# Performance work log

Measured on AMD Instinct MI355X. Metric: run time of the kernel, lower is better.

Reference implementation:

```python
import jax, jax.numpy as jnp
import numpy as np

NUM_GRAPHS = 4
N_NODES = 50000
N_EDGES = 800000
D_IN = 64
D_HID = 64
D_OUT = 64


def setup_inputs() -> dict:
    key = jax.random.key(0)
    ks = jax.random.split(key, 8)
    x = jax.random.normal(ks[0], (NUM_GRAPHS, N_NODES, D_IN), dtype=jnp.float32)
    edge_index = jax.random.randint(ks[1], (NUM_GRAPHS, 2, N_EDGES), 0, N_NODES, dtype=jnp.int64)
    s = 0.05
    W_l1 = jax.random.normal(ks[2], (NUM_GRAPHS, D_IN, D_HID), dtype=jnp.float32) * s
    W_r1 = jax.random.normal(ks[3], (NUM_GRAPHS, D_IN, D_HID), dtype=jnp.float32) * s
    b1 = jax.random.normal(ks[4], (NUM_GRAPHS, D_HID), dtype=jnp.float32) * s
    W_l2 = jax.random.normal(ks[5], (NUM_GRAPHS, D_HID, D_OUT), dtype=jnp.float32) * s
    W_r2 = jax.random.normal(ks[6], (NUM_GRAPHS, D_HID, D_OUT), dtype=jnp.float32) * s
    b2 = jax.random.normal(ks[7], (NUM_GRAPHS, D_OUT), dtype=jnp.float32) * s
    return {"x": x, "edge_index": edge_index, "W_l1": W_l1, "W_r1": W_r1,
            "b1": b1, "W_l2": W_l2, "W_r2": W_r2, "b2": b2}


def _sage_conv(x, src, dst, W_l, W_r, b):
    # PyG SAGEConv (aggr='mean', root_weight=True): mean(x[src] -> dst) @ W_l + b + x @ W_r
    n = x.shape[0]
    msgs = x[src]                                            # [E, d] irregular gather
    agg = jax.ops.segment_sum(msgs, dst, num_segments=n)     # [N, d]
    deg = jax.ops.segment_sum(jnp.ones((src.shape[0],), x.dtype), dst, num_segments=n)
    mean = agg / jnp.maximum(deg, 1.0)[:, None]              # empty neighborhoods -> 0
    return mean @ W_l + b + x @ W_r


def _per_graph(x, edge_index, W_l1, W_r1, b1, W_l2, W_r2, b2):
    src, dst = edge_index[0], edge_index[1]
    h = jax.nn.elu(_sage_conv(x, src, dst, W_l1, W_r1, b1))
    return jax.nn.elu(_sage_conv(h, src, dst, W_l2, W_r2, b2))


def reference(x, edge_index, W_l1, W_r1, b1, W_l2, W_r2, b2):
    out = jax.vmap(_per_graph)(x, edge_index, W_l1, W_r1, b1, W_l2, W_r2, b2)  # [G, N, out]
    return out.reshape(-1, out.shape[-1])  # concat along node dim -> [G*N, out]
```

## Files before the change

kernel.cpp:

```cpp
#include <hip/hip_runtime.h>
#include <hip/hip_bf16.h>
#include <math.h>

#define NG 4
#define NN 50000
#define NE 800000
#define DD 64
#define CAP 64
#define NT 64
#define NTILE 391
#define NTG (2 * NTILE)
#define RCAP 1536
#define CPAD 16
#define PBLK 128
#define CHUNK (NE / PBLK)
#define LBINS 392
#define BCAP 20

typedef __attribute__((ext_vector_type(8))) short short8;
typedef __attribute__((ext_vector_type(4))) float float4v;

__device__ __forceinline__ unsigned short f2b(float f) {
    union { __hip_bfloat16 h; unsigned short u; } cv;
    cv.h = __float2bfloat16(f);
    return cv.u;
}
__device__ __forceinline__ float b2f(unsigned short u) {
    union { unsigned short u; __hip_bfloat16 h; } cv;
    cv.u = u;
    return __bfloat162float(cv.h);
}

__global__ void init_kernel(const int* __restrict__ ei, int* __restrict__ flags) {
    __shared__ alignas(16) unsigned short A[16 * 32];
    __shared__ unsigned short B[32 * 16];
    int t = threadIdx.x;
    int any_nonzero = 0;
    for (int i = t; i < 128; i += 64) any_nonzero |= ei[2 * i + 1];
    unsigned long long nz = __ballot(any_nonzero != 0);
    int is64 = (nz == 0ULL) ? 1 : 0;
    for (int i = t; i < 512; i += 64) {
        int r = i >> 5, k = i & 31;
        A[i] = f2b((float)(((r * 5 + k * 3) & 31) - 15));
        int kk = i >> 4, c = i & 15;
        B[i] = f2b((float)(((kk * 7 + c * 11) & 31) - 15));
    }
    __syncthreads();
    short8 a = *(const short8*)&A[(t & 15) * 32 + (t >> 4) * 8];
    int c = t & 15, kb = (t >> 4) * 8;
    short8 b;
    for (int j = 0; j < 8; ++j) b[j] = (short)B[(kb + j) * 16 + c];
    float4v acc = {0.f, 0.f, 0.f, 0.f};
    acc = __builtin_amdgcn_mfma_f32_16x16x32_bf16(a, b, acc, 0, 0, 0);
    int ok = 1;
    for (int reg = 0; reg < 4; ++reg) {
        int row = (t >> 4) * 4 + reg;
        float ref = 0.f;
        for (int k = 0; k < 32; ++k)
            ref += (float)(((row * 5 + k * 3) & 31) - 15) *
                   (float)(((k * 7 + c * 11) & 31) - 15);
        if (acc[reg] != ref) ok = 0;
    }
    unsigned long long vote = __ballot(ok);
    if (t == 0) flags[0] = is64 | ((vote == ~0ULL) ? 2 : 0);
}

__device__ __forceinline__ int nt_idx(const int* __restrict__ ei, long pos, int is64) {
    return is64 ? __builtin_nontemporal_load(ei + 2 * pos)
                : __builtin_nontemporal_load(ei + pos);
}

__global__ void partition_kernel(const int* __restrict__ ei, const int* __restrict__ flags,
                                 int* __restrict__ bcnt, unsigned int* __restrict__ part) {
    __shared__ int lcnt[LBINS];
    __shared__ int basev[LBINS];
    __shared__ unsigned int lbuf[LBINS * BCAP];

    int is64 = flags[0] & 1;
    int s = blockIdx.x & 7;
    int g = s >> 1;
    int lo = (s & 1) * (NN / 2), hi = lo + (NN / 2);
    int rbase0 = lo >> 6;
    int bsl = blockIdx.x >> 3;
    int e0 = bsl * CHUNK, e1 = e0 + CHUNK;
    long ebase = (long)g * 2 * NE;

    for (int i = threadIdx.x; i < LBINS; i += 256) lcnt[i] = 0;
    __syncthreads();

    for (int e = e0 + threadIdx.x; e < e1; e += 256) {
        int d = nt_idx(ei, ebase + NE + e, is64);
        int sc = nt_idx(ei, ebase + e, is64);
        if (d >= lo && d < hi) {
            int lb = (d >> 6) - rbase0;
            unsigned int pk = ((unsigned int)d << 16) | (unsigned int)(sc & 0xffff);
            int pos = atomicAdd(&lcnt[lb], 1);
            if (pos < BCAP) {
                lbuf[lb * BCAP + pos] = pk;
            } else {
                int gp = atomicAdd(&bcnt[(g * NTG + (d >> 6)) * CPAD], 1);
                if (gp < RCAP) part[(long)(g * NTG + (d >> 6)) * RCAP + gp] = pk;
            }
        }
    }
    __syncthreads();

    for (int r = threadIdx.x; r < LBINS; r += 256) {
        int c = lcnt[r]; c = c < BCAP ? c : BCAP;
        basev[r] = c ? atomicAdd(&bcnt[(g * NTG + rbase0 + r) * CPAD], c) : 0;
    }
    __syncthreads();

    int w = threadIdx.x >> 6, hw = (threadIdx.x >> 5) & 1, l32 = threadIdx.x & 31;
    for (int r = w * 2 + hw; r < LBINS; r += 8) {
        int c = lcnt[r]; c = c < BCAP ? c : BCAP;
        int b = basev[r];
        if (l32 < c && b + l32 < RCAP)
            part[(long)(g * NTG + rbase0 + r) * RCAP + b + l32] = lbuf[r * BCAP + l32];
    }
}

__global__ void convert_kernel(const float* __restrict__ x, unsigned short* __restrict__ xb) {
    long total = (long)NG * NN * DD / 4;
    long stride = (long)gridDim.x * blockDim.x;
    const float4* src = (const float4*)x;
    unsigned long long* dst = (unsigned long long*)xb;
    for (long i = (long)blockIdx.x * blockDim.x + threadIdx.x; i < total; i += stride) {
        float4 v = src[i];
        unsigned long long p = (unsigned long long)f2b(v.x)
                             | ((unsigned long long)f2b(v.y) << 16)
                             | ((unsigned long long)f2b(v.z) << 32)
                             | ((unsigned long long)f2b(v.w) << 48);
        dst[i] = p;
    }
}

template <int LAYER>
__launch_bounds__(256, 6)
__global__ void sage_mfma_kernel(const unsigned short* __restrict__ xin,
                                 const int* __restrict__ bcnt,
                                 const unsigned int* __restrict__ part,
                                 const float* __restrict__ Wl, const float* __restrict__ Wr,
                                 const float* __restrict__ bias, void* __restrict__ outp,
                                 const int* __restrict__ flags) {
    if (!(flags[0] & 2)) return;
    __shared__ alignas(16) unsigned short sWT[2 * DD * DD];
    __shared__ alignas(16) unsigned short sM[NT * DD];
    __shared__ int cnt_lds[NT];

    int s = blockIdx.x & 7, tb = blockIdx.x >> 3;
    int g = s >> 1;
    int tile = (s & 1) * NTILE + tb;
    int base = tile * NT;
    long gn0 = (long)g * NN;

    if (threadIdx.x < NT) cnt_lds[threadIdx.x] = 0;

    for (int i = threadIdx.x; i < 1024; i += 256) {
        int col = i & 63, ko = (i >> 6) & 7, m = i >> 9;
        const float* Wsrc = (m == 0 ? Wl : Wr) + (long)g * DD * DD;
        short8 t;
#pragma unroll
        for (int j = 0; j < 8; ++j)
            t[j] = (short)f2b(Wsrc[(ko * 8 + j) * DD + col]);
        *(short8*)&sWT[m * DD * DD + col * DD + ((ko * 8) ^ ((col & 7) << 3))] = t;
    }
    __syncthreads();

    int rc = bcnt[(g * NTG + tile) * CPAD];
    int rcount = rc < RCAP ? rc : RCAP;
    const unsigned int* reg = part + (long)(g * NTG + tile) * RCAP;
    for (int i = threadIdx.x; i < rcount; i += 256) {
        unsigned int p = reg[i];
        int dl = (p >> 16) & 63;
        int pos = atomicAdd(&cnt_lds[dl], 1);
        if (pos < CAP) sM[dl * DD + pos] = (unsigned short)(p & 0xffffu);
    }
    __syncthreads();

    int lane = threadIdx.x & 63;
    int w = threadIdx.x >> 6;

#pragma unroll 1
    for (int j = 0; j < 16; ++j) {
        int rl = w * 16 + j;
        int node = base + rl;
        int ne = cnt_lds[rl];
        int nuse = ne < CAP ? ne : CAP;
        int msrc = (int)sM[rl * DD + lane];
        float mean = 0.f;
        if (node < NN) {
            float s0 = 0.f, s1 = 0.f, s2 = 0.f, s3 = 0.f;
            int e = 0;
            for (; e + 4 <= nuse; e += 4) {
                int a0 = __shfl(msrc, e), a1 = __shfl(msrc, e + 1);
                int a2 = __shfl(msrc, e + 2), a3 = __shfl(msrc, e + 3);
                s0 += b2f(xin[(gn0 + a0) * DD + lane]);
                s1 += b2f(xin[(gn0 + a1) * DD + lane]);
                s2 += b2f(xin[(gn0 + a2) * DD + lane]);
                s3 += b2f(xin[(gn0 + a3) * DD + lane]);
            }
            if (e < nuse) {
                int r = nuse - e;
                int a0 = __shfl(msrc, e);
                int a1 = __shfl(msrc, r > 1 ? e + 1 : e);
                int a2 = __shfl(msrc, r > 2 ? e + 2 : e);
                float v0 = b2f(xin[(gn0 + a0) * DD + lane]);
                float v1 = b2f(xin[(gn0 + a1) * DD + lane]);
                float v2 = b2f(xin[(gn0 + a2) * DD + lane]);
                s0 += v0;
                if (r > 1) s1 += v1;
                if (r > 2) s2 += v2;
            }
            mean = ((s0 + s1) + (s2 + s3)) / fmaxf((float)ne, 1.f);
        }
        sM[rl * DD + (lane ^ ((rl & 7) << 3))] = f2b(mean);
    }

    int arow = w * 16 + (lane & 15);
    int kb = (lane >> 4) * 8;
    int selfrow = base + arow; if (selfrow > NN - 1) selfrow = NN - 1;
    short8 am[2], ax[2];
#pragma unroll
    for (int ss = 0; ss < 2; ++ss) {
        int f0 = (kb + 32 * ss) ^ ((arow & 7) << 3);
        am[ss] = *(const short8*)&sM[arow * DD + f0];
        ax[ss] = *(const short8*)&xin[(gn0 + selfrow) * DD + kb + 32 * ss];
    }

    float4v acc[4];
#pragma unroll
    for (int c = 0; c < 4; ++c) {
        float b = bias[g * DD + c * 16 + (lane & 15)];
        acc[c] = {b, b, b, b};
    }
#pragma unroll
    for (int c = 0; c < 4; ++c) {
        int col = c * 16 + (lane & 15);
        int cswz = (col & 7) << 3;
#pragma unroll
        for (int ss = 0; ss < 2; ++ss) {
            short8 bl = *(const short8*)&sWT[0 * DD * DD + col * DD + ((kb + 32 * ss) ^ cswz)];
            acc[c] = __builtin_amdgcn_mfma_f32_16x16x32_bf16(am[ss], bl, acc[c], 0, 0, 0);
        }
#pragma unroll
        for (int ss = 0; ss < 2; ++ss) {
            short8 br = *(const short8*)&sWT[1 * DD * DD + col * DD + ((kb + 32 * ss) ^ cswz)];
            acc[c] = __builtin_amdgcn_mfma_f32_16x16x32_bf16(ax[ss], br, acc[c], 0, 0, 0);
        }
    }

    int q = lane >> 4, cl = lane & 15;
#pragma unroll
    for (int c = 0; c < 4; ++c) {
        int col = c * 16 + cl;
#pragma unroll
        for (int r = 0; r < 4; ++r) {
            int grow = base + w * 16 + q * 4 + r;
            if (grow >= NN) continue;
            float v = acc[c][r];
            v = v > 0.f ? v : expm1f(v);
            if (LAYER == 0)
                ((unsigned short*)outp)[(gn0 + grow) * DD + col] = f2b(v);
            else
                ((float*)outp)[(gn0 + grow) * DD + col] = v;
        }
    }
}

template <int LAYER>
__global__ void fallback_kernel(const unsigned short* __restrict__ xin,
                                const int* __restrict__ bcnt,
                                const unsigned int* __restrict__ part,
                                const float* __restrict__ Wl, const float* __restrict__ Wr,
                                const float* __restrict__ bias, void* __restrict__ outp,
                                const int* __restrict__ flags) {
    if (flags[0] & 2) return;
    __shared__ float sWl[DD * DD];
    __shared__ float sWr[DD * DD];
    __shared__ float sb[DD];
    __shared__ unsigned short bk[NT * CAP];
    __shared__ int cnt_lds[NT];

    int s = blockIdx.x & 7, tb = blockIdx.x >> 3;
    int g = s >> 1;
    int tile = (s & 1) * NTILE + tb;
    int base = tile * NT;
    long gn0 = (long)g * NN;

    if (threadIdx.x < NT) cnt_lds[threadIdx.x] = 0;
    for (int i = threadIdx.x; i < DD * DD; i += blockDim.x) {
        sWl[i] = Wl[(long)g * DD * DD + i];
        sWr[i] = Wr[(long)g * DD * DD + i];
    }
    if (threadIdx.x < DD) sb[threadIdx.x] = bias[g * DD + threadIdx.x];
    __syncthreads();

    int rc = bcnt[(g * NTG + tile) * CPAD];
    int rcount = rc < RCAP ? rc : RCAP;
    const unsigned int* reg = part + (long)(g * NTG + tile) * RCAP;
    for (int i = threadIdx.x; i < rcount; i += 256) {
        unsigned int p = reg[i];
        int dl = (p >> 16) & 63;
        int pos = atomicAdd(&cnt_lds[dl], 1);
        if (pos < CAP) bk[dl * CAP + pos] = (unsigned short)(p & 0xffffu);
    }
    __syncthreads();

    int lane = threadIdx.x & 63;
    int w = threadIdx.x >> 6;
    for (int j = 0; j < 16; ++j) {
        int rl = w * 16 + j;
        int node = base + rl;
        if (node >= NN) continue;
        long row = gn0 + node;
        int ne = cnt_lds[rl];
        int nuse = ne < CAP ? ne : CAP;
        int msrc = (int)bk[rl * CAP + lane];
        float sum = 0.f;
        for (int e = 0; e < nuse; ++e) {
            int a0 = __shfl(msrc, e);
            sum += b2f(xin[(gn0 + a0) * DD + lane]);
        }
        float mean = sum / fmaxf((float)ne, 1.f);
        float self = b2f(xin[row * DD + lane]);
        float acc = sb[lane];
#pragma unroll
        for (int k = 0; k < DD; ++k) {
            float mk = __shfl(mean, k);
            float xk = __shfl(self, k);
            acc += mk * sWl[k * DD + lane] + xk * sWr[k * DD + lane];
        }
        acc = acc > 0.f ? acc : expm1f(acc);
        if (LAYER == 0) ((unsigned short*)outp)[row * DD + lane] = f2b(acc);
        else            ((float*)outp)[row * DD + lane] = acc;
    }
}

extern "C" void kernel_launch(void* const* d_in, const int* in_sizes, int n_in,
                              void* d_out, int out_size, void* d_ws, size_t ws_size,
                              hipStream_t stream) {
    const float* x   = (const float*)d_in[0];
    const int*   ei  = (const int*)d_in[1];
    const float* Wl1 = (const float*)d_in[2];
    const float* Wr1 = (const float*)d_in[3];
    const float* b1  = (const float*)d_in[4];
    const float* Wl2 = (const float*)d_in[5];
    const float* Wr2 = (const float*)d_in[6];
    const float* b2  = (const float*)d_in[7];
    float* out = (float*)d_out;

    unsigned int* part = (unsigned int*)d_ws;
    int* bcnt = (int*)(part + (size_t)NG * NTG * RCAP);
    unsigned short* h = (unsigned short*)(bcnt + (size_t)NG * NTG * CPAD);
    int* flags = (int*)(h + (size_t)NG * NN * DD);
    unsigned short* xb = (unsigned short*)d_out;

    hipMemsetAsync(bcnt, 0, (size_t)NG * NTG * CPAD * sizeof(int), stream);
    init_kernel<<<1, 64, 0, stream>>>(ei, flags);
    partition_kernel<<<PBLK * 8, 256, 0, stream>>>(ei, flags, bcnt, part);
    convert_kernel<<<2048, 256, 0, stream>>>(x, xb);

    const int grid = NTILE * 8;
    sage_mfma_kernel<0><<<grid, 256, 0, stream>>>(xb, bcnt, part, Wl1, Wr1, b1, h, flags);
    fallback_kernel<0><<<grid, 256, 0, stream>>>(xb, bcnt, part, Wl1, Wr1, b1, h, flags);
    sage_mfma_kernel<1><<<grid, 256, 0, stream>>>(h, bcnt, part, Wl2, Wr2, b2, out, flags);
    fallback_kernel<1><<<grid, 256, 0, stream>>>(h, bcnt, part, Wl2, Wr2, b2, out, flags);
}
```

Baseline: 302.5 us.

## Pre-swizzle bf16 weights once and gather 4 neighbors per wave with 8-byte loads

Adds a small kernel that converts both layers' weights to bf16 in the swizzled transposed layout once, so each block copies them into LDS with 16-byte loads instead of converting scattered fp32 reads. The neighbor gather is also restructured so each wave handles four edges at a time: each 16-lane group loads a full 128-byte row with 8-byte loads, and the partial sums are combined with cross-lane shuffles. This is meant to cut per-block weight preparation and the number of narrow 2-byte gather loads, at the cost of an extra launch, more workspace and shuffle reductions.

```diff
diff --git a/kernel.cpp b/kernel.cpp
--- a/kernel.cpp
+++ b/kernel.cpp
@@ -135,12 +135,26 @@
     }
 }
 
+__global__ void wconv_kernel(const float* __restrict__ Wl1, const float* __restrict__ Wr1,
+                             const float* __restrict__ Wl2, const float* __restrict__ Wr2,
+                             unsigned short* __restrict__ wsw) {
+    int g = blockIdx.x & 3, layer = blockIdx.x >> 2;
+    const float* Wl = layer ? Wl2 : Wl1;
+    const float* Wr = layer ? Wr2 : Wr1;
+    for (int i = threadIdx.x; i < 2 * DD * DD; i += 256) {
+        int m = i >> 12, rem = i & 4095, k = rem >> 6, col = rem & 63;
+        float wv = (m == 0 ? Wl : Wr)[(long)g * DD * DD + rem];
+        wsw[(((long)layer * NG + g) * 2 + m) * DD * DD + col * DD + (k ^ ((col & 7) << 3))]
+            = f2b(wv);
+    }
+}
+
 template <int LAYER>
 __launch_bounds__(256, 6)
 __global__ void sage_mfma_kernel(const unsigned short* __restrict__ xin,
                                  const int* __restrict__ bcnt,
                                  const unsigned int* __restrict__ part,
-                                 const float* __restrict__ Wl, const float* __restrict__ Wr,
+                                 const unsigned short* __restrict__ wsw,
                                  const float* __restrict__ bias, void* __restrict__ outp,
                                  const int* __restrict__ flags) {
     if (!(flags[0] & 2)) return;
@@ -156,14 +170,10 @@
 
     if (threadIdx.x < NT) cnt_lds[threadIdx.x] = 0;
 
-    for (int i = threadIdx.x; i < 1024; i += 256) {
-        int col = i & 63, ko = (i >> 6) & 7, m = i >> 9;
-        const float* Wsrc = (m == 0 ? Wl : Wr) + (long)g * DD * DD;
-        short8 t;
-#pragma unroll
-        for (int j = 0; j < 8; ++j)
-            t[j] = (short)f2b(Wsrc[(ko * 8 + j) * DD + col]);
-        *(short8*)&sWT[m * DD * DD + col * DD + ((ko * 8) ^ ((col & 7) << 3))] = t;
+    {
+        const short8* wsrc = (const short8*)(wsw + ((long)LAYER * NG + g) * 2 * DD * DD);
+        short8* wdst = (short8*)sWT;
+        for (int i = threadIdx.x; i < 1024; i += 256) wdst[i] = wsrc[i];
     }
     __syncthreads();
 
@@ -180,6 +190,9 @@
 
     int lane = threadIdx.x & 63;
     int w = threadIdx.x >> 6;
+    int grp = lane >> 4;
+    int fq  = lane & 15;
+    const char* xg = (const char*)xin + (gn0 << 7);
 
 #pragma unroll 1
     for (int j = 0; j < 16; ++j) {
@@ -188,33 +201,36 @@
         int ne = cnt_lds[rl];
         int nuse = ne < CAP ? ne : CAP;
         int msrc = (int)sM[rl * DD + lane];
-        float mean = 0.f;
-        if (node < NN) {
-            float s0 = 0.f, s1 = 0.f, s2 = 0.f, s3 = 0.f;
-            int e = 0;
-            for (; e + 4 <= nuse; e += 4) {
-                int a0 = __shfl(msrc, e), a1 = __shfl(msrc, e + 1);
-                int a2 = __shfl(msrc, e + 2), a3 = __shfl(msrc, e + 3);
-                s0 += b2f(xin[(gn0 + a0) * DD + lane]);
-                s1 += b2f(xin[(gn0 + a1) * DD + lane]);
-                s2 += b2f(xin[(gn0 + a2) * DD + lane]);
-                s3 += b2f(xin[(gn0 + a3) * DD + lane]);
+        float a0 = 0.f, a1 = 0.f, a2 = 0.f, a3 = 0.f;
+        if (node < NN && nuse > 0) {
+#pragma unroll 4
+            for (int e = 0; e < nuse; e += 4) {
+                int ei = e + grp;
+                bool valid = ei < nuse;
+                int srcv = __shfl(msrc, valid ? ei : 0);
+                unsigned long long v =
+                    *(const unsigned long long*)(xg + ((long)srcv << 7) + (fq << 3));
+                unsigned int u0 = (unsigned int)v, u1 = (unsigned int)(v >> 32);
+                if (!valid) { u0 = 0u; u1 = 0u; }
+                a0 += __uint_as_float(u0 << 16);
+                a1 += __uint_as_float(u0 & 0xffff0000u);
+                a2 += __uint_as_float(u1 << 16);
+                a3 += __uint_as_float(u1 & 0xffff0000u);
             }
-            if (e < nuse) {
-                int r = nuse - e;
-                int a0 = __shfl(msrc, e);
-                int a1 = __shfl(msrc, r > 1 ? e + 1 : e);
-                int a2 = __shfl(msrc, r > 2 ? e + 2 : e);
-                float v0 = b2f(xin[(gn0 + a0) * DD + lane]);
-                float v1 = b2f(xin[(gn0 + a1) * DD + lane]);
-                float v2 = b2f(xin[(gn0 + a2) * DD + lane]);
-                s0 += v0;
-                if (r > 1) s1 += v1;
-                if (r > 2) s2 += v2;
-            }
-            mean = ((s0 + s1) + (s2 + s3)) / fmaxf((float)ne, 1.f);
-        }
-        sM[rl * DD + (lane ^ ((rl & 7) << 3))] = f2b(mean);
+            a0 += __shfl_xor(a0, 16); a0 += __shfl_xor(a0, 32);
+            a1 += __shfl_xor(a1, 16); a1 += __shfl_xor(a1, 32);
+            a2 += __shfl_xor(a2, 16); a2 += __shfl_xor(a2, 32);
+            a3 += __shfl_xor(a3, 16); a3 += __shfl_xor(a3, 32);
+            float inv = 1.f / fmaxf((float)ne, 1.f);
+            a0 *= inv; a1 *= inv; a2 *= inv; a3 *= inv;
+        }
+        unsigned int p0 = (unsigned int)f2b(a0) | ((unsigned int)f2b(a1) << 16);
+        unsigned int p1 = (unsigned int)f2b(a2) | ((unsigned int)f2b(a3) << 16);
+        if (grp == 0) {
+            int swz = (fq * 4) ^ ((rl & 7) << 3);
+            *(unsigned long long*)&sM[rl * DD + swz] =
+                ((unsigned long long)p1 << 32) | (unsigned long long)p0;
+        }
     }
 
     int arow = w * 16 + (lane & 15);
@@ -353,17 +369,19 @@
     unsigned int* part = (unsigned int*)d_ws;
     int* bcnt = (int*)(part + (size_t)NG * NTG * RCAP);
     unsigned short* h = (unsigned short*)(bcnt + (size_t)NG * NTG * CPAD);
-    int* flags = (int*)(h + (size_t)NG * NN * DD);
+    unsigned short* wsw = h + (size_t)NG * NN * DD;
+    int* flags = (int*)(wsw + (size_t)2 * NG * 2 * DD * DD);
     unsigned short* xb = (unsigned short*)d_out;
 
     hipMemsetAsync(bcnt, 0, (size_t)NG * NTG * CPAD * sizeof(int), stream);
     init_kernel<<<1, 64, 0, stream>>>(ei, flags);
     partition_kernel<<<PBLK * 8, 256, 0, stream>>>(ei, flags, bcnt, part);
     convert_kernel<<<2048, 256, 0, stream>>>(x, xb);
+    wconv_kernel<<<8, 256, 0, stream>>>(Wl1, Wr1, Wl2, Wr2, wsw);
 
     const int grid = NTILE * 8;
-    sage_mfma_kernel<0><<<grid, 256, 0, stream>>>(xb, bcnt, part, Wl1, Wr1, b1, h, flags);
+    sage_mfma_kernel<0><<<grid, 256, 0, stream>>>(xb, bcnt, part, wsw, b1, h, flags);
     fallback_kernel<0><<<grid, 256, 0, stream>>>(xb, bcnt, part, Wl1, Wr1, b1, h, flags);
-    sage_mfma_kernel<1><<<grid, 256, 0, stream>>>(h, bcnt, part, Wl2, Wr2, b2, out, flags);
+    sage_mfma_kernel<1><<<grid, 256, 0, stream>>>(h, bcnt, part, wsw, b2, out, flags);
     fallback_kernel<1><<<grid, 256, 0, stream>>>(h, bcnt, part, Wl2, Wr2, b2, out, flags);
 }
```

New measurement: 319.4 us. +5.6%, slower.
